# Optimization experiments

Measured on AMD Instinct MI355X. Metric: run time of the kernel, lower is better.

## Reference

```python
import jax, jax.numpy as jnp
import numpy as np

EMBED = 1024
HEADS = 16
HEAD_DIM = EMBED // HEADS
FF = 4 * EMBED
B, S = 2, 2048


def setup_inputs() -> dict:
    key = jax.random.key(0)
    ks = jax.random.split(key, 16)
    sd = 0.02
    inp = {
        "x": jax.random.normal(ks[0], (B, S, EMBED), dtype=jnp.float32),
        "Wq": jax.random.normal(ks[1], (EMBED, EMBED), dtype=jnp.float32) * sd,
        "bq": jnp.zeros((EMBED,), jnp.float32),
        "Wk": jax.random.normal(ks[2], (EMBED, EMBED), dtype=jnp.float32) * sd,
        "bk": jnp.zeros((EMBED,), jnp.float32),
        "Wv": jax.random.normal(ks[3], (EMBED, EMBED), dtype=jnp.float32) * sd,
        "bv": jnp.zeros((EMBED,), jnp.float32),
        "Wo": jax.random.normal(ks[4], (EMBED, EMBED), dtype=jnp.float32) * sd,
        "W1": jax.random.normal(ks[5], (EMBED, FF), dtype=jnp.float32) * sd,
        "b1": jnp.zeros((FF,), jnp.float32),
        "W2": jax.random.normal(ks[6], (FF, EMBED), dtype=jnp.float32) * sd,
        "b2": jnp.zeros((EMBED,), jnp.float32),
        "g1": jnp.ones((EMBED,), jnp.float32),
        "be1": jnp.zeros((EMBED,), jnp.float32),
        "g2": jnp.ones((EMBED,), jnp.float32),
        "be2": jnp.zeros((EMBED,), jnp.float32),
    }
    return inp


def _layernorm(x, g, b, eps=1e-5):
    mu = jnp.mean(x, axis=-1, keepdims=True)
    var = jnp.mean(jnp.square(x - mu), axis=-1, keepdims=True)
    return (x - mu) * jax.lax.rsqrt(var + eps) * g + b


def _attn(x, Wq, bq, Wk, bk, Wv, bv, Wo):
    b, s, d = x.shape
    q = (x @ Wq + bq).reshape(b, s, HEADS, HEAD_DIM)
    k = (x @ Wk + bk).reshape(b, s, HEADS, HEAD_DIM)
    v = (x @ Wv + bv).reshape(b, s, HEADS, HEAD_DIM)
    # NOTE: original scales by sqrt(embed_dim), NOT sqrt(head_dim)
    logits = jnp.einsum('bqhd,bkhd->bhqk', q, k) / jnp.sqrt(jnp.float32(d))
    mask = jnp.tril(jnp.ones((s, s), dtype=bool))
    logits = jnp.where(mask, logits, -jnp.inf)
    w = jax.nn.softmax(logits, axis=-1)
    z = jnp.einsum('bhqk,bkhd->bqhd', w, v).reshape(b, s, d)
    return z @ Wo


def reference(x, Wq, bq, Wk, bk, Wv, bv, Wo, W1, b1, W2, b2, g1, be1, g2, be2):
    h = x + _attn(_layernorm(x, g1, be1), Wq, bq, Wk, bk, Wv, bv, Wo)
    m = _layernorm(h, g2, be2)
    m = jax.nn.gelu(m @ W1 + b1, approximate=False) @ W2 + b2
    return h + m
```

## Files before the change

### kernel.cpp

```cpp
#include <hip/hip_runtime.h>
#include <cstdint>
#include <cstddef>
#include <math.h>

#define EMBED 1024
#define SEQ   2048
#define NROWS 4096
#define NHEADS 16

typedef __bf16 bf16x8 __attribute__((ext_vector_type(8)));
typedef float f32x4 __attribute__((ext_vector_type(4)));
typedef unsigned short us8 __attribute__((ext_vector_type(8)));
typedef unsigned short us4 __attribute__((ext_vector_type(4)));

__device__ __forceinline__ unsigned short f2bf(float f) {
  union { float f; unsigned u; } v; v.f = f;
  unsigned r = v.u + 0x7fffu + ((v.u >> 16) & 1u);
  return (unsigned short)(r >> 16);
}
__device__ __forceinline__ float bf2f(unsigned short u) {
  union { unsigned u; float f; } v; v.u = (unsigned)u << 16; return v.f;
}

__device__ __forceinline__ bf16x8 as_bf(us8 u) { return __builtin_bit_cast(bf16x8, u); }

__device__ __forceinline__ void gload_lds16(const unsigned short* g, unsigned short* l) {
  __builtin_amdgcn_global_load_lds((const __attribute__((address_space(1))) void*)g,
                                   (__attribute__((address_space(3))) void*)l, 16, 0, 0);
}

__global__ __launch_bounds__(256) void transpose_to_bf16(
    const float* __restrict__ in, unsigned short* __restrict__ out, int K, int N) {
  __shared__ float tile[32][33];
  const int tx = threadIdx.x & 31, ty = threadIdx.x >> 5;
  const int n0 = blockIdx.x * 32, k0 = blockIdx.y * 32;
#pragma unroll
  for (int i = 0; i < 4; i++) {
    int k = ty + i * 8;
    tile[k][tx] = in[(size_t)(k0 + k) * N + n0 + tx];
  }
  __syncthreads();
#pragma unroll
  for (int i = 0; i < 4; i++) {
    int n = ty + i * 8;
    out[(size_t)(n0 + n) * K + k0 + tx] = f2bf(tile[tx][n]);
  }
}

__global__ __launch_bounds__(256) void layernorm_bf16(
    const float* __restrict__ x, const float* __restrict__ g,
    const float* __restrict__ be, unsigned short* __restrict__ out) {
  const int wave = threadIdx.x >> 6, lane = threadIdx.x & 63;
  const int row = blockIdx.x * 4 + wave;
  const float* xr = x + (size_t)row * EMBED;
  float4 v[4];
  float s = 0.f, sq = 0.f;
#pragma unroll
  for (int c = 0; c < 4; c++) {
    v[c] = *(const float4*)&xr[c * 256 + lane * 4];
    s  += v[c].x + v[c].y + v[c].z + v[c].w;
    sq += v[c].x * v[c].x + v[c].y * v[c].y + v[c].z * v[c].z + v[c].w * v[c].w;
  }
#pragma unroll
  for (int m = 1; m < 64; m <<= 1) {
    s  += __shfl_xor(s, m, 64);
    sq += __shfl_xor(sq, m, 64);
  }
  const float mean = s * (1.f / 1024.f);
  const float var  = sq * (1.f / 1024.f) - mean * mean;
  const float rstd = rsqrtf(var + 1e-5f);
#pragma unroll
  for (int c = 0; c < 4; c++) {
    const int idx = c * 256 + lane * 4;
    us4 o;
    o[0] = f2bf((v[c].x - mean) * rstd * g[idx + 0] + be[idx + 0]);
    o[1] = f2bf((v[c].y - mean) * rstd * g[idx + 1] + be[idx + 1]);
    o[2] = f2bf((v[c].z - mean) * rstd * g[idx + 2] + be[idx + 2]);
    o[3] = f2bf((v[c].w - mean) * rstd * g[idx + 3] + be[idx + 3]);
    *(us4*)&out[(size_t)row * EMBED + idx] = o;
  }
}

__global__ __launch_bounds__(256) void ln2_fused(
    const float* __restrict__ x,
    const unsigned short* __restrict__ pw0,
    const unsigned short* __restrict__ pw1,
    const float* __restrict__ g, const float* __restrict__ be,
    float* __restrict__ hb, unsigned short* __restrict__ out) {
  const int wave = threadIdx.x >> 6, lane = threadIdx.x & 63;
  const int row = blockIdx.x * 4 + wave;
  const size_t rb = (size_t)row * EMBED;
  float4 v[4];
  float s = 0.f, sq = 0.f;
#pragma unroll
  for (int c = 0; c < 4; c++) {
    const int idx = c * 256 + lane * 4;
    const float4 xv = *(const float4*)&x[rb + idx];
    const us4 a = *(const us4*)&pw0[rb + idx];
    const us4 d = *(const us4*)&pw1[rb + idx];
    v[c].x = xv.x + bf2f(a[0]) + bf2f(d[0]);
    v[c].y = xv.y + bf2f(a[1]) + bf2f(d[1]);
    v[c].z = xv.z + bf2f(a[2]) + bf2f(d[2]);
    v[c].w = xv.w + bf2f(a[3]) + bf2f(d[3]);
    *(float4*)&hb[rb + idx] = v[c];
    s  += v[c].x + v[c].y + v[c].z + v[c].w;
    sq += v[c].x * v[c].x + v[c].y * v[c].y + v[c].z * v[c].z + v[c].w * v[c].w;
  }
#pragma unroll
  for (int m = 1; m < 64; m <<= 1) {
    s  += __shfl_xor(s, m, 64);
    sq += __shfl_xor(sq, m, 64);
  }
  const float mean = s * (1.f / 1024.f);
  const float var  = sq * (1.f / 1024.f) - mean * mean;
  const float rstd = rsqrtf(var + 1e-5f);
#pragma unroll
  for (int c = 0; c < 4; c++) {
    const int idx = c * 256 + lane * 4;
    us4 o;
    o[0] = f2bf((v[c].x - mean) * rstd * g[idx + 0] + be[idx + 0]);
    o[1] = f2bf((v[c].y - mean) * rstd * g[idx + 1] + be[idx + 1]);
    o[2] = f2bf((v[c].z - mean) * rstd * g[idx + 2] + be[idx + 2]);
    o[3] = f2bf((v[c].w - mean) * rstd * g[idx + 3] + be[idx + 3]);
    *(us4*)&out[rb + idx] = o;
  }
}

enum { MODE_QKV = 0, MODE_WO = 1, MODE_FF1 = 2, MODE_FF2 = 3, MODE_PART = 4 };

template <int MODE>
__global__ __launch_bounds__(256) void gemm_bf16(
    const unsigned short* __restrict__ A,
    const unsigned short* __restrict__ Bt0,
    const unsigned short* __restrict__ Bt1,
    const unsigned short* __restrict__ Bt2,
    const float* __restrict__ bias0,
    const float* __restrict__ bias1,
    const float* __restrict__ bias2,
    const float* __restrict__ res,
    void* __restrict__ out0, void* __restrict__ out1,
    void* __restrict__ out2, void* __restrict__ out3,
    int M, int N, int K) {
  const unsigned short* Bt = Bt0;
  const float* bias = bias0;
  void* outv = out0;
  int zidx = 0;
  if constexpr (MODE == MODE_QKV) {
    zidx = blockIdx.z;
    if (zidx == 1)      { Bt = Bt1; bias = bias1; outv = out1; }
    else if (zidx == 2) { Bt = Bt2; bias = bias2; outv = out2; }
  }
  if constexpr (MODE == MODE_PART) {
    zidx = blockIdx.z;
    outv = (zidx == 0) ? out0 : (zidx == 1) ? out1 : (zidx == 2) ? out2 : out3;
  }
  const int Ksub = (MODE == MODE_PART) ? K / (int)gridDim.z : K;
  const int koff = (MODE == MODE_PART) ? zidx * Ksub : 0;

  __shared__ unsigned short As[128 * 32];
  __shared__ unsigned short Bs[128 * 32];
  const int tid = threadIdx.x;
  const int wave = tid >> 6, lane = tid & 63;
  const int quad = lane >> 4, l15 = lane & 15;
  const int wr = (wave >> 1) * 64, wc = (wave & 1) * 64;
  const int rowA0 = blockIdx.y * 128, colB0 = blockIdx.x * 128;

  const int srow = tid >> 2;
  const int scol = (tid & 3) * 8;
  const unsigned short* gA = A  + (size_t)(rowA0 + srow) * K + koff + scol;
  const unsigned short* gB = Bt + (size_t)(colB0 + srow) * K + koff + scol;
  unsigned short* lA  = &As[tid * 8];
  unsigned short* lA2 = &As[2048 + tid * 8];
  unsigned short* lB  = &Bs[tid * 8];
  unsigned short* lB2 = &Bs[2048 + tid * 8];
  const size_t half = (size_t)64 * K;

  f32x4 acc[4][4];
#pragma unroll
  for (int i = 0; i < 4; i++)
#pragma unroll
    for (int j = 0; j < 4; j++) acc[i][j] = f32x4{0.f, 0.f, 0.f, 0.f};

  for (int k0 = 0; k0 < Ksub; k0 += 32) {
    gload_lds16(gA + k0, lA);
    gload_lds16(gA + half + k0, lA2);
    gload_lds16(gB + k0, lB);
    gload_lds16(gB + half + k0, lB2);
    __syncthreads();
    bf16x8 af[4], bfr[4];
#pragma unroll
    for (int mi = 0; mi < 4; mi++)
      af[mi] = as_bf(*(const us8*)&As[(wr + mi * 16 + l15) * 32 + quad * 8]);
#pragma unroll
    for (int ni = 0; ni < 4; ni++)
      bfr[ni] = as_bf(*(const us8*)&Bs[(wc + ni * 16 + l15) * 32 + quad * 8]);
#pragma unroll
    for (int mi = 0; mi < 4; mi++)
#pragma unroll
      for (int ni = 0; ni < 4; ni++)
        acc[mi][ni] = __builtin_amdgcn_mfma_f32_16x16x32_bf16(af[mi], bfr[ni], acc[mi][ni], 0, 0, 0);
    __syncthreads();
  }

#pragma unroll
  for (int ni = 0; ni < 4; ni++) {
    const int col = colB0 + wc + ni * 16 + l15;
    float bv = 0.f;
    if constexpr (MODE == MODE_QKV || MODE == MODE_FF1 || MODE == MODE_FF2) bv = bias[col];
#pragma unroll
    for (int mi = 0; mi < 4; mi++) {
      const int row0 = rowA0 + wr + mi * 16 + quad * 4;
      if constexpr (MODE == MODE_QKV) {
        unsigned short* o = (unsigned short*)outv;
        if (zidx == 2) {
          us4 pk;
#pragma unroll
          for (int r = 0; r < 4; r++) pk[r] = f2bf(acc[mi][ni][r] + bv);
          const int bb = row0 >> 11;
          const int sr = row0 & 2047;
          *(us4*)&o[((size_t)(bb * 1024 + col)) * SEQ + sr] = pk;
        } else {
#pragma unroll
          for (int r = 0; r < 4; r++)
            o[(size_t)(row0 + r) * N + col] = f2bf(acc[mi][ni][r] + bv);
        }
      } else if constexpr (MODE == MODE_FF1) {
        unsigned short* o = (unsigned short*)outv;
#pragma unroll
        for (int r = 0; r < 4; r++) {
          float v = acc[mi][ni][r] + bv;
          v = 0.5f * v * (1.f + erff(v * 0.7071067811865476f));
          o[(size_t)(row0 + r) * N + col] = f2bf(v);
        }
      } else if constexpr (MODE == MODE_PART) {
        unsigned short* o = (unsigned short*)outv;
#pragma unroll
        for (int r = 0; r < 4; r++)
          o[(size_t)(row0 + r) * N + col] = f2bf(acc[mi][ni][r]);
      } else {
        float* o = (float*)outv;
#pragma unroll
        for (int r = 0; r < 4; r++) {
          float v = acc[mi][ni][r] + bv + res[(size_t)(row0 + r) * N + col];
          o[(size_t)(row0 + r) * N + col] = v;
        }
      }
    }
  }
}

__global__ __launch_bounds__(256) void ff2_reduce(
    const float* __restrict__ hb, const float* __restrict__ b2,
    const unsigned short* __restrict__ p0, const unsigned short* __restrict__ p1,
    const unsigned short* __restrict__ p2, const unsigned short* __restrict__ p3,
    float* __restrict__ out) {
  const size_t i = ((size_t)blockIdx.x * 256 + threadIdx.x) * 4;
  const int col = (int)(i & (EMBED - 1));
  const float4 h = *(const float4*)&hb[i];
  const float4 bb = *(const float4*)&b2[col];
  const us4 a = *(const us4*)&p0[i];
  const us4 b = *(const us4*)&p1[i];
  const us4 c = *(const us4*)&p2[i];
  const us4 d = *(const us4*)&p3[i];
  float4 o;
  o.x = h.x + bb.x + bf2f(a[0]) + bf2f(b[0]) + bf2f(c[0]) + bf2f(d[0]);
  o.y = h.y + bb.y + bf2f(a[1]) + bf2f(b[1]) + bf2f(c[1]) + bf2f(d[1]);
  o.z = h.z + bb.z + bf2f(a[2]) + bf2f(b[2]) + bf2f(c[2]) + bf2f(d[2]);
  o.w = h.w + bb.w + bf2f(a[3]) + bf2f(b[3]) + bf2f(c[3]) + bf2f(d[3]);
  *(float4*)&out[i] = o;
}

__global__ __launch_bounds__(256) void attn_kernel(
    const unsigned short* __restrict__ Q,
    const unsigned short* __restrict__ Kb,
    const unsigned short* __restrict__ Vt,
    unsigned short* __restrict__ Z) {
  __shared__ unsigned short Ksh[64][72];
  __shared__ unsigned short Vsh[64][72];
  __shared__ unsigned short Pt[4][16][72];
  __shared__ float Ot[4][64][17];

  const int tid = threadIdx.x;
  const int wave = tid >> 6, lane = tid & 63;
  const int quad = lane >> 4, l15 = lane & 15;
  const int bh = blockIdx.x, b = bh >> 4, h = bh & 15;
  const float cscale = 1.4426950408889634f / 32.f;

  const int srow = tid >> 2;
  const int sc = (tid & 3) * 8;
  const unsigned short* Kbase = Kb + (size_t)(b * SEQ) * EMBED + h * 64;
  const unsigned short* Vbase = Vt + (size_t)(b * 1024 + h * 64) * SEQ;

#pragma unroll
  for (int ph = 0; ph < 2; ph++) {
    const int j = ph ? 31 - (int)blockIdx.y : (int)blockIdx.y;
    const int qc = j * 64 + wave * 16;

    bf16x8 qf[2];
#pragma unroll
    for (int kf = 0; kf < 2; kf++)
      qf[kf] = as_bf(*(const us8*)&Q[(size_t)(b * SEQ + qc + l15) * EMBED +
                                     h * 64 + kf * 32 + quad * 8]);

    f32x4 accO[4];
#pragma unroll
    for (int dt = 0; dt < 4; dt++) accO[dt] = f32x4{0.f, 0.f, 0.f, 0.f};
    float mrun = -INFINITY, lrun = 0.f;

    for (int kt = 0; kt <= j; kt++) {
      const int kbase = kt * 64;
      const unsigned short* kg = Kbase + (size_t)(kbase + srow) * EMBED + sc;
      const unsigned short* vg = Vbase + (size_t)srow * SEQ + kbase + sc;
      const us8 k0 = *(const us8*)kg;
      const us8 k1 = *(const us8*)(kg + 32);
      const us8 v0 = *(const us8*)vg;
      const us8 v1 = *(const us8*)(vg + 32);
      __syncthreads();
      *(us8*)&Ksh[srow][sc]      = k0;
      *(us8*)&Ksh[srow][32 + sc] = k1;
      *(us8*)&Vsh[srow][sc]      = v0;
      *(us8*)&Vsh[srow][32 + sc] = v1;
      __syncthreads();

      f32x4 sf[4];
#pragma unroll
      for (int nt = 0; nt < 4; nt++) {
        f32x4 z4 = f32x4{0.f, 0.f, 0.f, 0.f};
#pragma unroll
        for (int kf = 0; kf < 2; kf++) {
          const bf16x8 ka = as_bf(*(const us8*)&Ksh[nt * 16 + l15][kf * 32 + quad * 8]);
          z4 = __builtin_amdgcn_mfma_f32_16x16x32_bf16(ka, qf[kf], z4, 0, 0, 0);
        }
        sf[nt] = z4 * cscale;
      }
      if (kt == j) {
        const int q = qc + l15;
#pragma unroll
        for (int nt = 0; nt < 4; nt++) {
          const int key0 = kbase + nt * 16 + quad * 4;
#pragma unroll
          for (int r = 0; r < 4; r++)
            if (key0 + r > q) sf[nt][r] = -INFINITY;
        }
      }
      float mx = sf[0][0];
#pragma unroll
      for (int nt = 0; nt < 4; nt++)
#pragma unroll
        for (int r = 0; r < 4; r++) mx = fmaxf(mx, sf[nt][r]);
      mx = fmaxf(mx, __shfl_xor(mx, 16, 64));
      mx = fmaxf(mx, __shfl_xor(mx, 32, 64));
      const float mnew = fmaxf(mrun, mx);
      const float alpha = exp2f(mrun - mnew);
      mrun = mnew;
      float rs = 0.f;
#pragma unroll
      for (int nt = 0; nt < 4; nt++) {
        us4 pk;
#pragma unroll
        for (int r = 0; r < 4; r++) {
          const float p = exp2f(sf[nt][r] - mnew);
          rs += p;
          pk[r] = f2bf(p);
        }
        *(us4*)&Pt[wave][l15][nt * 16 + quad * 4] = pk;
      }
      rs += __shfl_xor(rs, 16, 64);
      rs += __shfl_xor(rs, 32, 64);
      lrun = lrun * alpha + rs;
#pragma unroll
      for (int dt = 0; dt < 4; dt++) accO[dt] = accO[dt] * alpha;
      bf16x8 pf[2];
#pragma unroll
      for (int kk = 0; kk < 2; kk++)
        pf[kk] = as_bf(*(const us8*)&Pt[wave][l15][kk * 32 + quad * 8]);
#pragma unroll
      for (int dt = 0; dt < 4; dt++)
#pragma unroll
        for (int kk = 0; kk < 2; kk++) {
          const bf16x8 va = as_bf(*(const us8*)&Vsh[dt * 16 + l15][kk * 32 + quad * 8]);
          accO[dt] = __builtin_amdgcn_mfma_f32_16x16x32_bf16(va, pf[kk], accO[dt], 0, 0, 0);
        }
    }

    const float inv = 1.f / lrun;
#pragma unroll
    for (int dt = 0; dt < 4; dt++)
#pragma unroll
      for (int r = 0; r < 4; r++)
        Ot[wave][dt * 16 + quad * 4 + r][l15] = accO[dt][r] * inv;
    const int lq = lane >> 2, dbase = (lane & 3) * 16;
    us8 o0, o1;
#pragma unroll
    for (int i = 0; i < 8; i++) o0[i] = f2bf(Ot[wave][dbase + i][lq]);
#pragma unroll
    for (int i = 0; i < 8; i++) o1[i] = f2bf(Ot[wave][dbase + 8 + i][lq]);
    unsigned short* zp = Z + (size_t)(b * SEQ + qc + lq) * EMBED + h * 64 + dbase;
    *(us8*)zp = o0;
    *(us8*)(zp + 8) = o1;
  }
}

extern "C" void kernel_launch(void* const* d_in, const int* in_sizes, int n_in,
                              void* d_out, int out_size, void* d_ws, size_t ws_size,
                              hipStream_t stream) {
  const float* x   = (const float*)d_in[0];
  const float* Wq  = (const float*)d_in[1];
  const float* bq  = (const float*)d_in[2];
  const float* Wk  = (const float*)d_in[3];
  const float* bk  = (const float*)d_in[4];
  const float* Wv  = (const float*)d_in[5];
  const float* bv  = (const float*)d_in[6];
  const float* Wo  = (const float*)d_in[7];
  const float* W1  = (const float*)d_in[8];
  const float* b1  = (const float*)d_in[9];
  const float* W2  = (const float*)d_in[10];
  const float* b2  = (const float*)d_in[11];
  const float* g1  = (const float*)d_in[12];
  const float* be1 = (const float*)d_in[13];
  const float* g2  = (const float*)d_in[14];
  const float* be2 = (const float*)d_in[15];
  float* out = (float*)d_out;

  char* ws = (char*)d_ws;
  const size_t MB = 1024 * 1024;
  unsigned short* wqT = (unsigned short*)(ws + 0 * MB);
  unsigned short* wkT = (unsigned short*)(ws + 2 * MB);
  unsigned short* wvT = (unsigned short*)(ws + 4 * MB);
  unsigned short* woT = (unsigned short*)(ws + 6 * MB);
  unsigned short* w1T = (unsigned short*)(ws + 8 * MB);
  unsigned short* w2T = (unsigned short*)(ws + 16 * MB);
  unsigned short* ln1 = (unsigned short*)(ws + 24 * MB);
  unsigned short* zb  = (unsigned short*)(ws + 24 * MB);
  unsigned short* ln2 = (unsigned short*)(ws + 24 * MB);
  unsigned short* p2  = (unsigned short*)(ws + 24 * MB);
  unsigned short* qb  = (unsigned short*)(ws + 32 * MB);
  unsigned short* kb2 = (unsigned short*)(ws + 40 * MB);
  float*          hb  = (float*)         (ws + 32 * MB);
  unsigned short* vT  = (unsigned short*)(ws + 48 * MB);
  unsigned short* pw0 = (unsigned short*)(ws + 48 * MB);
  unsigned short* p3  = (unsigned short*)(ws + 48 * MB);
  unsigned short* pw1 = (unsigned short*)(ws + 56 * MB);
  unsigned short* m1  = (unsigned short*)(ws + 56 * MB);
  unsigned short* p0  = (unsigned short*)(ws + 0 * MB);
  unsigned short* p1  = (unsigned short*)(ws + 8 * MB);
  (void)in_sizes; (void)n_in; (void)out_size; (void)ws_size;

  transpose_to_bf16<<<dim3(32, 32), 256, 0, stream>>>(Wq, wqT, 1024, 1024);
  transpose_to_bf16<<<dim3(32, 32), 256, 0, stream>>>(Wk, wkT, 1024, 1024);
  transpose_to_bf16<<<dim3(32, 32), 256, 0, stream>>>(Wv, wvT, 1024, 1024);
  transpose_to_bf16<<<dim3(32, 32), 256, 0, stream>>>(Wo, woT, 1024, 1024);
  transpose_to_bf16<<<dim3(128, 32), 256, 0, stream>>>(W1, w1T, 1024, 4096);
  transpose_to_bf16<<<dim3(32, 128), 256, 0, stream>>>(W2, w2T, 4096, 1024);

  layernorm_bf16<<<NROWS / 4, 256, 0, stream>>>(x, g1, be1, ln1);

  gemm_bf16<MODE_QKV><<<dim3(8, 32, 3), 256, 0, stream>>>(
      ln1, wqT, wkT, wvT, bq, bk, bv, nullptr, qb, kb2, vT, nullptr,
      NROWS, 1024, 1024);

  attn_kernel<<<dim3(32, 16), 256, 0, stream>>>(qb, kb2, vT, zb);

  gemm_bf16<MODE_PART><<<dim3(8, 32, 2), 256, 0, stream>>>(
      zb, woT, nullptr, nullptr, nullptr, nullptr, nullptr, nullptr,
      pw0, pw1, nullptr, nullptr, NROWS, 1024, 1024);

  ln2_fused<<<NROWS / 4, 256, 0, stream>>>(x, pw0, pw1, g2, be2, hb, ln2);

  gemm_bf16<MODE_FF1><<<dim3(32, 32), 256, 0, stream>>>(
      ln2, w1T, nullptr, nullptr, b1, nullptr, nullptr, nullptr,
      m1, nullptr, nullptr, nullptr, NROWS, 4096, 1024);

  gemm_bf16<MODE_PART><<<dim3(8, 32, 4), 256, 0, stream>>>(
      m1, w2T, nullptr, nullptr, nullptr, nullptr, nullptr, nullptr,
      p0, p1, p2, p3, NROWS, 1024, 4096);

  ff2_reduce<<<NROWS * EMBED / (256 * 4), 256, 0, stream>>>(
      hb, b2, p0, p1, p2, p3, out);
}
```

Baseline: 416.0 us.

## Register-prefetch GEMM tiles and pad LDS rows to avoid bank conflicts

Replaces the direct global-to-LDS loads in the bf16 GEMM with register staging. The next K-tile is fetched into registers while the current tile is consumed by MFMA. LDS rows are padded from 32 to 36 elements to reduce bank conflicts on the fragment reads. This costs extra VGPRs and LDS, and the loop still has two barriers per iteration.

```diff
diff --git a/kernel.cpp b/kernel.cpp
--- a/kernel.cpp
+++ b/kernel.cpp
@@ -23,11 +23,6 @@
 }
 
 __device__ __forceinline__ bf16x8 as_bf(us8 u) { return __builtin_bit_cast(bf16x8, u); }
-
-__device__ __forceinline__ void gload_lds16(const unsigned short* g, unsigned short* l) {
-  __builtin_amdgcn_global_load_lds((const __attribute__((address_space(1))) void*)g,
-                                   (__attribute__((address_space(3))) void*)l, 16, 0, 0);
-}
 
 __global__ __launch_bounds__(256) void transpose_to_bf16(
     const float* __restrict__ in, unsigned short* __restrict__ out, int K, int N) {
@@ -127,6 +122,8 @@
 }
 
 enum { MODE_QKV = 0, MODE_WO = 1, MODE_FF1 = 2, MODE_FF2 = 3, MODE_PART = 4 };
+
+#define LDW 36
 
 template <int MODE>
 __global__ __launch_bounds__(256) void gemm_bf16(
@@ -157,8 +154,8 @@
   const int Ksub = (MODE == MODE_PART) ? K / (int)gridDim.z : K;
   const int koff = (MODE == MODE_PART) ? zidx * Ksub : 0;
 
-  __shared__ unsigned short As[128 * 32];
-  __shared__ unsigned short Bs[128 * 32];
+  __shared__ unsigned short As[128 * LDW];
+  __shared__ unsigned short Bs[128 * LDW];
   const int tid = threadIdx.x;
   const int wave = tid >> 6, lane = tid & 63;
   const int quad = lane >> 4, l15 = lane & 15;
@@ -169,12 +166,13 @@
   const int scol = (tid & 3) * 8;
   const unsigned short* gA = A  + (size_t)(rowA0 + srow) * K + koff + scol;
   const unsigned short* gB = Bt + (size_t)(colB0 + srow) * K + koff + scol;
-  unsigned short* lA  = &As[tid * 8];
-  unsigned short* lA2 = &As[2048 + tid * 8];
-  unsigned short* lB  = &Bs[tid * 8];
-  unsigned short* lB2 = &Bs[2048 + tid * 8];
   const size_t half = (size_t)64 * K;
 
+  us8 ra0 = *(const us8*)gA;
+  us8 ra1 = *(const us8*)(gA + half);
+  us8 rb0 = *(const us8*)gB;
+  us8 rb1 = *(const us8*)(gB + half);
+
   f32x4 acc[4][4];
 #pragma unroll
   for (int i = 0; i < 4; i++)
@@ -182,24 +180,30 @@
     for (int j = 0; j < 4; j++) acc[i][j] = f32x4{0.f, 0.f, 0.f, 0.f};
 
   for (int k0 = 0; k0 < Ksub; k0 += 32) {
-    gload_lds16(gA + k0, lA);
-    gload_lds16(gA + half + k0, lA2);
-    gload_lds16(gB + k0, lB);
-    gload_lds16(gB + half + k0, lB2);
+    __syncthreads();
+    *(us8*)&As[srow * LDW + scol]        = ra0;
+    *(us8*)&As[(srow + 64) * LDW + scol] = ra1;
+    *(us8*)&Bs[srow * LDW + scol]        = rb0;
+    *(us8*)&Bs[(srow + 64) * LDW + scol] = rb1;
+    if (k0 + 32 < Ksub) {
+      ra0 = *(const us8*)(gA + k0 + 32);
+      ra1 = *(const us8*)(gA + half + k0 + 32);
+      rb0 = *(const us8*)(gB + k0 + 32);
+      rb1 = *(const us8*)(gB + half + k0 + 32);
+    }
     __syncthreads();
     bf16x8 af[4], bfr[4];
 #pragma unroll
     for (int mi = 0; mi < 4; mi++)
-      af[mi] = as_bf(*(const us8*)&As[(wr + mi * 16 + l15) * 32 + quad * 8]);
+      af[mi] = as_bf(*(const us8*)&As[(wr + mi * 16 + l15) * LDW + quad * 8]);
 #pragma unroll
     for (int ni = 0; ni < 4; ni++)
-      bfr[ni] = as_bf(*(const us8*)&Bs[(wc + ni * 16 + l15) * 32 + quad * 8]);
+      bfr[ni] = as_bf(*(const us8*)&Bs[(wc + ni * 16 + l15) * LDW + quad * 8]);
 #pragma unroll
     for (int mi = 0; mi < 4; mi++)
 #pragma unroll
       for (int ni = 0; ni < 4; ni++)
         acc[mi][ni] = __builtin_amdgcn_mfma_f32_16x16x32_bf16(af[mi], bfr[ni], acc[mi][ni], 0, 0, 0);
-    __syncthreads();
   }
 
 #pragma unroll
```

New measurement: 389.2 us. 1.07x faster.

## Software-pipeline GEMM loads with register prefetch and double-buffered padded LDS

Applied to the files above, without the earlier changes.

Replaces the direct global-to-LDS loads and two barriers per k-step in the GEMM with a three-stage register prefetch feeding a double-buffered LDS tile. The LDS row stride is padded to avoid bank conflicts, and the trip count becomes a compile-time template parameter so the loop fully unrolls. The six weight transpose launches are also merged into one kernel to cut launch overhead. The cost is more registers for the prefetch buffers, which may lower occupancy, and a full unroll that grows code size.

```diff
diff --git a/kernel.cpp b/kernel.cpp
--- a/kernel.cpp
+++ b/kernel.cpp
@@ -24,16 +24,32 @@
 
 __device__ __forceinline__ bf16x8 as_bf(us8 u) { return __builtin_bit_cast(bf16x8, u); }
 
-__device__ __forceinline__ void gload_lds16(const unsigned short* g, unsigned short* l) {
-  __builtin_amdgcn_global_load_lds((const __attribute__((address_space(1))) void*)g,
-                                   (__attribute__((address_space(3))) void*)l, 16, 0, 0);
-}
-
-__global__ __launch_bounds__(256) void transpose_to_bf16(
-    const float* __restrict__ in, unsigned short* __restrict__ out, int K, int N) {
+__global__ __launch_bounds__(256) void transpose_all(
+    const float* __restrict__ Wq, const float* __restrict__ Wk,
+    const float* __restrict__ Wv, const float* __restrict__ Wo,
+    const float* __restrict__ W1, const float* __restrict__ W2,
+    unsigned short* __restrict__ wqT, unsigned short* __restrict__ wkT,
+    unsigned short* __restrict__ wvT, unsigned short* __restrict__ woT,
+    unsigned short* __restrict__ w1T, unsigned short* __restrict__ w2T) {
   __shared__ float tile[32][33];
+  const int bid = blockIdx.x;
+  const float* in;
+  unsigned short* out;
+  int K, N, bx, by;
+  if (bid < 4096) {
+    const int w = bid >> 10, t = bid & 1023;
+    in  = (w == 0) ? Wq  : (w == 1) ? Wk  : (w == 2) ? Wv  : Wo;
+    out = (w == 0) ? wqT : (w == 1) ? wkT : (w == 2) ? wvT : woT;
+    K = 1024; N = 1024; bx = t & 31; by = t >> 5;
+  } else if (bid < 8192) {
+    const int t = bid - 4096;
+    in = W1; out = w1T; K = 1024; N = 4096; bx = t & 127; by = t >> 7;
+  } else {
+    const int t = bid - 8192;
+    in = W2; out = w2T; K = 4096; N = 1024; bx = t & 31; by = t >> 5;
+  }
   const int tx = threadIdx.x & 31, ty = threadIdx.x >> 5;
-  const int n0 = blockIdx.x * 32, k0 = blockIdx.y * 32;
+  const int n0 = bx * 32, k0 = by * 32;
 #pragma unroll
   for (int i = 0; i < 4; i++) {
     int k = ty + i * 8;
@@ -128,7 +144,9 @@
 
 enum { MODE_QKV = 0, MODE_WO = 1, MODE_FF1 = 2, MODE_FF2 = 3, MODE_PART = 4 };
 
-template <int MODE>
+#define LDW 36
+
+template <int MODE, int NITER>
 __global__ __launch_bounds__(256) void gemm_bf16(
     const unsigned short* __restrict__ A,
     const unsigned short* __restrict__ Bt0,
@@ -154,11 +172,10 @@
     zidx = blockIdx.z;
     outv = (zidx == 0) ? out0 : (zidx == 1) ? out1 : (zidx == 2) ? out2 : out3;
   }
-  const int Ksub = (MODE == MODE_PART) ? K / (int)gridDim.z : K;
-  const int koff = (MODE == MODE_PART) ? zidx * Ksub : 0;
-
-  __shared__ unsigned short As[128 * 32];
-  __shared__ unsigned short Bs[128 * 32];
+  const int koff = (MODE == MODE_PART) ? zidx * (NITER * 32) : 0;
+
+  __shared__ unsigned short As[2][128 * LDW];
+  __shared__ unsigned short Bs[2][128 * LDW];
   const int tid = threadIdx.x;
   const int wave = tid >> 6, lane = tid & 63;
   const int quad = lane >> 4, l15 = lane & 15;
@@ -169,37 +186,60 @@
   const int scol = (tid & 3) * 8;
   const unsigned short* gA = A  + (size_t)(rowA0 + srow) * K + koff + scol;
   const unsigned short* gB = Bt + (size_t)(colB0 + srow) * K + koff + scol;
-  unsigned short* lA  = &As[tid * 8];
-  unsigned short* lA2 = &As[2048 + tid * 8];
-  unsigned short* lB  = &Bs[tid * 8];
-  unsigned short* lB2 = &Bs[2048 + tid * 8];
   const size_t half = (size_t)64 * K;
 
+  us8 pa0[3], pa1[3], pb0[3], pb1[3];
+#pragma unroll
+  for (int s = 0; s < 3; s++) {
+    if (s < NITER) {
+      pa0[s] = *(const us8*)(gA + s * 32);
+      pa1[s] = *(const us8*)(gA + half + s * 32);
+      pb0[s] = *(const us8*)(gB + s * 32);
+      pb1[s] = *(const us8*)(gB + half + s * 32);
+    }
+  }
+  *(us8*)&As[0][srow * LDW + scol]        = pa0[0];
+  *(us8*)&As[0][(srow + 64) * LDW + scol] = pa1[0];
+  *(us8*)&Bs[0][srow * LDW + scol]        = pb0[0];
+  *(us8*)&Bs[0][(srow + 64) * LDW + scol] = pb1[0];
+  __syncthreads();
+
   f32x4 acc[4][4];
 #pragma unroll
   for (int i = 0; i < 4; i++)
 #pragma unroll
     for (int j = 0; j < 4; j++) acc[i][j] = f32x4{0.f, 0.f, 0.f, 0.f};
 
-  for (int k0 = 0; k0 < Ksub; k0 += 32) {
-    gload_lds16(gA + k0, lA);
-    gload_lds16(gA + half + k0, lA2);
-    gload_lds16(gB + k0, lB);
-    gload_lds16(gB + half + k0, lB2);
-    __syncthreads();
+#pragma unroll
+  for (int k = 0; k < NITER; k++) {
+    const int buf = k & 1;
+    if (k + 1 < NITER) {
+      const int s = (k + 1) % 3;
+      *(us8*)&As[buf ^ 1][srow * LDW + scol]        = pa0[s];
+      *(us8*)&As[buf ^ 1][(srow + 64) * LDW + scol] = pa1[s];
+      *(us8*)&Bs[buf ^ 1][srow * LDW + scol]        = pb0[s];
+      *(us8*)&Bs[buf ^ 1][(srow + 64) * LDW + scol] = pb1[s];
+    }
+    if (k + 3 < NITER) {
+      const int s = k % 3;
+      pa0[s] = *(const us8*)(gA + (size_t)(k + 3) * 32);
+      pa1[s] = *(const us8*)(gA + half + (size_t)(k + 3) * 32);
+      pb0[s] = *(const us8*)(gB + (size_t)(k + 3) * 32);
+      pb1[s] = *(const us8*)(gB + half + (size_t)(k + 3) * 32);
+    }
     bf16x8 af[4], bfr[4];
 #pragma unroll
     for (int mi = 0; mi < 4; mi++)
-      af[mi] = as_bf(*(const us8*)&As[(wr + mi * 16 + l15) * 32 + quad * 8]);
+      af[mi] = as_bf(*(const us8*)&As[buf][(wr + mi * 16 + l15) * LDW + quad * 8]);
 #pragma unroll
     for (int ni = 0; ni < 4; ni++)
-      bfr[ni] = as_bf(*(const us8*)&Bs[(wc + ni * 16 + l15) * 32 + quad * 8]);
+      bfr[ni] = as_bf(*(const us8*)&Bs[buf][(wc + ni * 16 + l15) * LDW + quad * 8]);
 #pragma unroll
     for (int mi = 0; mi < 4; mi++)
 #pragma unroll
       for (int ni = 0; ni < 4; ni++)
         acc[mi][ni] = __builtin_amdgcn_mfma_f32_16x16x32_bf16(af[mi], bfr[ni], acc[mi][ni], 0, 0, 0);
-    __syncthreads();
+    if (k + 1 < NITER) __syncthreads();
   }
 
 #pragma unroll
@@ -446,32 +486,28 @@
   unsigned short* p1  = (unsigned short*)(ws + 8 * MB);
   (void)in_sizes; (void)n_in; (void)out_size; (void)ws_size;
 
-  transpose_to_bf16<<<dim3(32, 32), 256, 0, stream>>>(Wq, wqT, 1024, 1024);
-  transpose_to_bf16<<<dim3(32, 32), 256, 0, stream>>>(Wk, wkT, 1024, 1024);
-  transpose_to_bf16<<<dim3(32, 32), 256, 0, stream>>>(Wv, wvT, 1024, 1024);
-  transpose_to_bf16<<<dim3(32, 32), 256, 0, stream>>>(Wo, woT, 1024, 1024);
-  transpose_to_bf16<<<dim3(128, 32), 256, 0, stream>>>(W1, w1T, 1024, 4096);
-  transpose_to_bf16<<<dim3(32, 128), 256, 0, stream>>>(W2, w2T, 4096, 1024);
+  transpose_all<<<12288, 256, 0, stream>>>(Wq, Wk, Wv, Wo, W1, W2,
+                                           wqT, wkT, wvT, woT, w1T, w2T);
 
   layernorm_bf16<<<NROWS / 4, 256, 0, stream>>>(x, g1, be1, ln1);
 
-  gemm_bf16<MODE_QKV><<<dim3(8, 32, 3), 256, 0, stream>>>(
+  gemm_bf16<MODE_QKV, 32><<<dim3(8, 32, 3), 256, 0, stream>>>(
       ln1, wqT, wkT, wvT, bq, bk, bv, nullptr, qb, kb2, vT, nullptr,
       NROWS, 1024, 1024);
 
   attn_kernel<<<dim3(32, 16), 256, 0, stream>>>(qb, kb2, vT, zb);
 
-  gemm_bf16<MODE_PART><<<dim3(8, 32, 2), 256, 0, stream>>>(
+  gemm_bf16<MODE_PART, 16><<<dim3(8, 32, 2), 256, 0, stream>>>(
       zb, woT, nullptr, nullptr, nullptr, nullptr, nullptr, nullptr,
       pw0, pw1, nullptr, nullptr, NROWS, 1024, 1024);
 
   ln2_fused<<<NROWS / 4, 256, 0, stream>>>(x, pw0, pw1, g2, be2, hb, ln2);
 
-  gemm_bf16<MODE_FF1><<<dim3(32, 32), 256, 0, stream>>>(
+  gemm_bf16<MODE_FF1, 32><<<dim3(32, 32), 256, 0, stream>>>(
       ln2, w1T, nullptr, nullptr, b1, nullptr, nullptr, nullptr,
       m1, nullptr, nullptr, nullptr, NROWS, 4096, 1024);
 
-  gemm_bf16<MODE_PART><<<dim3(8, 32, 4), 256, 0, stream>>>(
+  gemm_bf16<MODE_PART, 32><<<dim3(8, 32, 4), 256, 0, stream>>>(
       m1, w2T, nullptr, nullptr, nullptr, nullptr, nullptr, nullptr,
       p0, p1, p2, p3, NROWS, 1024, 4096);
 
```

New measurement: 379.0 us. 1.1x faster.
